# Kernel tuning notes

Measured on AMD Instinct MI355X. Metric: run time of the kernel, lower is better.

## Reference

```python
import jax, jax.numpy as jnp
import numpy as np

B, D, N, H = 16, 512, 4096, 4
HD = D // H  # head_dim = 128


def conv1(x, w, b):
    # 1x1 Conv1d == per-position matmul. x: (b, Cin, L), w: (Cout, Cin), b: (Cout,)
    return jnp.einsum('oi,bin->bon', w, x) + b[:, None]


def ln_c(x, g, b, eps=1e-5):
    # TransLN: LayerNorm over the channel axis (axis=1) at every position.
    m = jnp.mean(x, axis=1, keepdims=True)
    v = jnp.var(x, axis=1, keepdims=True)
    return (x - m) * jax.lax.rsqrt(v + eps) * g[:, None] + b[:, None]


def gelu(x):
    return jax.nn.gelu(x, approximate=False)  # torch nn.GELU default = exact erf


def setup_inputs() -> dict:
    key = jax.random.key(0)
    ks = iter(jax.random.split(key, 40))

    def rn(*shape):
        return jax.random.normal(next(ks), shape, jnp.float32) * 0.02

    inp = {
        'group_token': jax.random.normal(next(ks), (B, D, 2), jnp.float32),
        'x': jax.random.normal(next(ks), (B, D, N), jnp.float32),
        # mlp_s: Mlp(2, D//2) -> Conv1d(2, D//2), GELU, Conv1d(D//2, 2)
        'ws1_w': rn(D // 2, 2), 'ws1_b': jnp.zeros(D // 2, jnp.float32),
        'ws2_w': rn(2, D // 2), 'ws2_b': jnp.zeros(2, jnp.float32),
        # mlp_c: Mlp(D, 4D)
        'wc1_w': rn(4 * D, D), 'wc1_b': jnp.zeros(4 * D, jnp.float32),
        'wc2_w': rn(D, 4 * D), 'wc2_b': jnp.zeros(D, jnp.float32),
        # proj q/k/v: Conv1d(D, D)
        'q_w': rn(D, D), 'q_b': jnp.zeros(D, jnp.float32),
        'k_w': rn(D, D), 'k_b': jnp.zeros(D, jnp.float32),
        'v_w': rn(D, D), 'v_b': jnp.zeros(D, jnp.float32),
        'merge_w': rn(D, D), 'merge_b': jnp.zeros(D, jnp.float32),
        # mlp = MLP([2D, 2D, D], do_bn=False): Conv1d(2D,2D), GELU, Conv1d(2D,D)
        'm1_w': rn(2 * D, 2 * D), 'm1_b': jnp.zeros(2 * D, jnp.float32),
        'm2_w': rn(D, 2 * D), 'm2_b': jnp.zeros(D, jnp.float32),
        # norm0 / norm1 LayerNorm(D)
        'n0_g': jnp.ones(D, jnp.float32), 'n0_b': jnp.zeros(D, jnp.float32),
        'n1_g': jnp.ones(D, jnp.float32), 'n1_b': jnp.zeros(D, jnp.float32),
        # grouping: D->64->16->4->2 with TransLN+GELU between, softmax(axis=1)
        'g1_w': rn(64, D), 'g1_b': jnp.zeros(64, jnp.float32),
        'gl1_g': jnp.ones(64, jnp.float32), 'gl1_b': jnp.zeros(64, jnp.float32),
        'g2_w': rn(16, 64), 'g2_b': jnp.zeros(16, jnp.float32),
        'gl2_g': jnp.ones(16, jnp.float32), 'gl2_b': jnp.zeros(16, jnp.float32),
        'g3_w': rn(4, 16), 'g3_b': jnp.zeros(4, jnp.float32),
        'gl3_g': jnp.ones(4, jnp.float32), 'gl3_b': jnp.zeros(4, jnp.float32),
        'g4_w': rn(2, 4), 'g4_b': jnp.zeros(2, jnp.float32),
    }
    return inp


def reference(group_token, x, ws1_w, ws1_b, ws2_w, ws2_b, wc1_w, wc1_b, wc2_w, wc2_b,
              q_w, q_b, k_w, k_b, v_w, v_b, merge_w, merge_b,
              m1_w, m1_b, m2_w, m2_b, n0_g, n0_b, n1_g, n1_b,
              g1_w, g1_b, gl1_g, gl1_b, g2_w, g2_b, gl2_g, gl2_b,
              g3_w, g3_b, gl3_g, gl3_b, g4_w, g4_b):
    b = x.shape[0]
    # group_token: (b, D, 2)
    gt_t = jnp.swapaxes(group_token, 1, 2)                    # (b, 2, D)
    s = conv1(gelu(conv1(gt_t, ws1_w, ws1_b)), ws2_w, ws2_b)  # (b, 2, D)
    gt = group_token + jnp.swapaxes(s, 1, 2)
    gt = gt + conv1(gelu(conv1(gt, wc1_w, wc1_b)), wc2_w, wc2_b)

    # projections; torch view(b, head_dim, heads, -1) splits channels as (HD, H)
    q = conv1(x, q_w, q_b).reshape(b, HD, H, N)
    k = conv1(gt, k_w, k_b).reshape(b, HD, H, 2)
    v = conv1(gt, v_w, v_b).reshape(b, HD, H, 2)

    attn = jax.nn.softmax(jnp.einsum('bdhn,bdhm->bhnm', q, k) * (HD ** -0.5), axis=-1)
    out = jnp.einsum('bhnm,bdhm->bdhn', attn, v).reshape(b, D, N)
    out = conv1(out, merge_w, merge_b)

    h = jnp.concatenate([x, ln_c(out, n0_g, n0_b)], axis=1)   # (b, 2D, N)
    h = conv1(gelu(conv1(h, m1_w, m1_b)), m2_w, m2_b)         # (b, D, N)
    xd = x + ln_c(h, n1_g, n1_b)

    g = gelu(ln_c(conv1(xd, g1_w, g1_b), gl1_g, gl1_b))
    g = gelu(ln_c(conv1(g, g2_w, g2_b), gl2_g, gl2_b))
    g = gelu(ln_c(conv1(g, g3_w, g3_b), gl3_g, gl3_b))
    g = jax.nn.softmax(conv1(g, g4_w, g4_b), axis=1)          # (b, 2, N)
    return g[:, 0, :]                                         # (b, N)
```

## Files before the change

kernel.cpp:

```cpp
#include <hip/hip_runtime.h>
#include <math.h>

typedef unsigned short u16;
typedef unsigned int u32;
typedef __attribute__((ext_vector_type(8))) short bfrag;
typedef __attribute__((ext_vector_type(4))) float f32x4;

__device__ __forceinline__ float gelu_f(float x){
  float z = fabsf(x) * 0.70710678118654752440f;
  float t = __builtin_amdgcn_rcpf(1.0f + 0.3275911f*z);
  float p = t*(0.254829592f + t*(-0.284496736f + t*(1.421413741f
            + t*(-1.453152027f + t*1.061405429f))));
  float e = __expf(-z*z);
  float er = copysignf(1.0f - p*e, x);
  return 0.5f * x * (1.0f + er);
}
__device__ __forceinline__ u16 f2bf(float f){
  union { float f; unsigned int i; } c; c.f = f;
  unsigned int i = c.i;
  return (u16)((i + 0x7FFFu + ((i >> 16) & 1u)) >> 16);
}
__device__ __forceinline__ float bf2f(u16 u){
  union { unsigned int i; float f; } c; c.i = ((unsigned int)u) << 16; return c.f;
}

__device__ __forceinline__ void gload_lds16(const u16* g, u16* l){
  __builtin_amdgcn_global_load_lds(
      (const __attribute__((address_space(1))) u32*)(g),
      (__attribute__((address_space(3))) u32*)(l),
      16, 0, 0);
}

struct F8 { float v[8]; };
__device__ __forceinline__ F8 load8f(const float* p){
  float4 a = *(const float4*)p; float4 b = *(const float4*)(p + 4);
  F8 r; r.v[0]=a.x; r.v[1]=a.y; r.v[2]=a.z; r.v[3]=a.w;
  r.v[4]=b.x; r.v[5]=b.y; r.v[6]=b.z; r.v[7]=b.w; return r;
}

#define PRE_STRIDE 4624

__global__ __launch_bounds__(256) void k0a_mlps(
    const float* __restrict__ gtok,
    const float* __restrict__ ws1_w, const float* __restrict__ ws1_b,
    const float* __restrict__ ws2_w, const float* __restrict__ ws2_b,
    float* __restrict__ GT1)
{
  __shared__ float sw1[256][2]; __shared__ float sb1[256];
  __shared__ float sw2[2][256];
  const int b = blockIdx.x;
  const int t = threadIdx.x;
  sw1[t][0] = ws1_w[2*t]; sw1[t][1] = ws1_w[2*t+1];
  sb1[t] = ws1_b[t];
  sw2[0][t] = ws2_w[t]; sw2[1][t] = ws2_w[256+t];
  __syncthreads();
  const int j = blockIdx.y*256 + t;
  const float a0 = gtok[b*1024 + 2*j], a1 = gtok[b*1024 + 2*j + 1];
  float s0 = ws2_b[0], s1 = ws2_b[1];
  #pragma unroll 4
  for (int o = 0; o < 256; ++o){
    float h = gelu_f(sw1[o][0]*a0 + sw1[o][1]*a1 + sb1[o]);
    s0 += sw2[0][o]*h; s1 += sw2[1][o]*h;
  }
  GT1[b*1024 + 2*j]     = a0 + s0;
  GT1[b*1024 + 2*j + 1] = a1 + s1;
}

__global__ __launch_bounds__(256) void k0b_fc1(
    const float* __restrict__ GT1,
    const float* __restrict__ wc1_w, const float* __restrict__ wc1_b,
    float* __restrict__ HID)
{
  __shared__ float g[1024];
  const int b = blockIdx.x;
  const int t = threadIdx.x;
  for (int i = t; i < 1024; i += 256) g[i] = GT1[b*1024 + i];
  __syncthreads();
  const int o = blockIdx.y*256 + t;
  const float* wr = wc1_w + (size_t)o*512;
  float acc0 = wc1_b[o], acc1 = acc0;
  for (int d = 0; d < 512; d += 8){
    F8 w = load8f(wr + d);
    #pragma unroll
    for (int i = 0; i < 8; ++i){
      acc0 += w.v[i]*g[(d+i)*2];
      acc1 += w.v[i]*g[(d+i)*2+1];
    }
  }
  HID[b*4096 + o]        = gelu_f(acc0);
  HID[b*4096 + 2048 + o] = gelu_f(acc1);
}

__global__ __launch_bounds__(256) void k0c_fc2(
    const float* __restrict__ GT1, const float* __restrict__ HID,
    const float* __restrict__ wc2_w, const float* __restrict__ wc2_b,
    float* __restrict__ GT2)
{
  __shared__ float h0[2048], h1[2048];
  const int b = blockIdx.x;
  const int t = threadIdx.x;
  for (int i = t; i < 2048; i += 256){
    h0[i] = HID[b*4096 + i]; h1[i] = HID[b*4096 + 2048 + i];
  }
  __syncthreads();
  const int d = blockIdx.y*256 + t;
  const float* wr = wc2_w + (size_t)d*2048;
  float acc0 = wc2_b[d], acc1 = acc0;
  for (int o = 0; o < 2048; o += 8){
    F8 w = load8f(wr + o);
    #pragma unroll
    for (int i = 0; i < 8; ++i){
      acc0 += w.v[i]*h0[o+i];
      acc1 += w.v[i]*h1[o+i];
    }
  }
  GT2[b*1024 + 2*d]     = GT1[b*1024 + 2*d]     + acc0;
  GT2[b*1024 + 2*d + 1] = GT1[b*1024 + 2*d + 1] + acc1;
}

__global__ __launch_bounds__(256) void k0d_kv(
    const float* __restrict__ GT2,
    const float* __restrict__ k_w,
    const float* __restrict__ v_w, const float* __restrict__ v_b,
    float* __restrict__ DK, float* __restrict__ DV, float* __restrict__ V1L)
{
  __shared__ float g[1024];
  const int b = blockIdx.x;
  const int t = threadIdx.x;
  for (int i = t; i < 1024; i += 256) g[i] = GT2[b*1024 + i];
  __syncthreads();
  const int c = blockIdx.y*256 + t;
  const float* kr = k_w + (size_t)c*512;
  const float* vr = v_w + (size_t)c*512;
  float k0a=0.f,k1a=0.f,v0a=0.f,v1a=0.f;
  for (int d = 0; d < 512; d += 8){
    F8 kw = load8f(kr + d); F8 vw = load8f(vr + d);
    #pragma unroll
    for (int i = 0; i < 8; ++i){
      float g0 = g[(d+i)*2], g1 = g[(d+i)*2+1];
      k0a += kw.v[i]*g0; k1a += kw.v[i]*g1;
      v0a += vw.v[i]*g0; v1a += vw.v[i]*g1;
    }
  }
  DK[b*512 + c]  = k0a - k1a;
  DV[b*512 + c]  = v0a - v1a;
  V1L[b*512 + c] = v1a + v_b[c];
}

__global__ __launch_bounds__(256) void k0e_qpre(
    const float* __restrict__ DK,
    const float* __restrict__ q_w, const float* __restrict__ q_b,
    float* __restrict__ PRE)
{
  __shared__ float dkl[512];
  const int b = blockIdx.x;
  const int t = threadIdx.x;
  for (int i = t; i < 512; i += 256) dkl[i] = DK[b*512 + i];
  __syncthreads();
  const int i = blockIdx.y*256 + t;
  float w0=0.f,w1=0.f,w2=0.f,w3=0.f;
  for (int c = 0; c < 512; c += 4){
    w0 += dkl[c]  *q_w[(size_t)(c)  *512 + i];
    w1 += dkl[c+1]*q_w[(size_t)(c+1)*512 + i];
    w2 += dkl[c+2]*q_w[(size_t)(c+2)*512 + i];
    w3 += dkl[c+3]*q_w[(size_t)(c+3)*512 + i];
  }
  float* P = PRE + (size_t)b * PRE_STRIDE;
  P[0*512+i]=w0; P[1*512+i]=w1; P[2*512+i]=w2; P[3*512+i]=w3;
  if (blockIdx.y == 0 && t < 4){
    float bsum = 0.f;
    for (int c = t; c < 512; c += 4) bsum += dkl[c]*q_b[c];
    P[2048 + t] = bsum;
  }
}

__global__ __launch_bounds__(256) void k0f_mpre(
    const float* __restrict__ DV, const float* __restrict__ V1L,
    const float* __restrict__ merge_w, const float* __restrict__ merge_b,
    float* __restrict__ PRE)
{
  __shared__ float dvl[512], v1ll[512];
  const int b = blockIdx.x;
  const int t = threadIdx.x;
  for (int i = t; i < 512; i += 256){
    dvl[i] = DV[b*512 + i]; v1ll[i] = V1L[b*512 + i];
  }
  __syncthreads();
  const int r = blockIdx.y*256 + t;
  const float* mw = merge_w + (size_t)r*512;
  float ab = merge_b[r];
  float mh[4] = {0.f,0.f,0.f,0.f};
  for (int c = 0; c < 512; c += 8){
    F8 w = load8f(mw + c);
    #pragma unroll
    for (int i = 0; i < 8; ++i){
      ab += w.v[i]*v1ll[c+i];
      mh[i&3] += w.v[i]*dvl[c+i];
    }
  }
  float* P = PRE + (size_t)b * PRE_STRIDE;
  P[2064 + r] = ab;
  *(float4*)&P[2576 + r*4] = make_float4(mh[0],mh[1],mh[2],mh[3]);
}

__global__ __launch_bounds__(256) void kcvt(const float* __restrict__ s,
                                            u16* __restrict__ d, int n8)
{
  int g = blockIdx.x*256 + threadIdx.x;
  if (g >= n8) return;
  F8 v = load8f(s + (size_t)g*8);
  u16 o[8];
  #pragma unroll
  for (int i=0;i<8;++i) o[i] = f2bf(v.v[i]);
  *(uint4*)(d + (size_t)g*8) = *(uint4*)o;
}

__global__ __launch_bounds__(256) void kcvt_dup(const float* __restrict__ g1w,
                                                u16* __restrict__ out)
{
  int idx = blockIdx.x*256 + threadIdx.x;
  int r = idx >> 10, k = idx & 1023;
  out[idx] = f2bf(g1w[r*512 + (k & 511)]);
}

__global__ __launch_bounds__(256) void k1_fused(
    const float* __restrict__ x, const float* __restrict__ PRE,
    const float* __restrict__ n0_g, const float* __restrict__ n0_b,
    int j0_global, u16* __restrict__ XYbT)
{
  __shared__ float wd[4][512];
  __shared__ float bs[512];
  __shared__ float Mm[512][4];
  __shared__ float gam[512], bet[512];
  __shared__ float beta4[4];
  __shared__ float part[4][4][64];
  __shared__ float pstat[2][4][64];
  const int tid = threadIdx.x;
  const int cid = tid & 63;
  const int qtr = tid >> 6;
  const int jl = blockIdx.x*64 + cid;
  const int jg = j0_global + jl;
  const int b = jg >> 12, n = jg & 4095;
  const float* P = PRE + (size_t)b * PRE_STRIDE;
  for (int i = tid; i < 2048; i += 256) wd[i>>9][i&511] = P[i];
  if (tid < 4) beta4[tid] = P[2048 + tid];
  for (int i = tid; i < 512; i += 256){
    bs[i] = P[2064 + i]; gam[i] = n0_g[i]; bet[i] = n0_b[i];
  }
  for (int i = tid; i < 2048; i += 256) Mm[i>>2][i&3] = P[2576 + i];
  __syncthreads();
  const float* xc = x + (size_t)b*2097152 + n;
  u16* col = XYbT + (size_t)jl*1024;
  const int ibase = qtr*128;
  float l0=0.f, l1=0.f, l2=0.f, l3=0.f;
  for (int i0 = 0; i0 < 128; i0 += 32){
    u16 ob[32];
    #pragma unroll
    for (int m = 0; m < 32; ++m){
      int i = ibase + i0 + m;
      float xv = xc[(size_t)i*4096];
      ob[m] = f2bf(xv);
      l0 += wd[0][i]*xv; l1 += wd[1][i]*xv;
      l2 += wd[2][i]*xv; l3 += wd[3][i]*xv;
    }
    #pragma unroll
    for (int q = 0; q < 4; ++q)
      *(uint4*)&col[ibase + i0 + 8*q] = *(uint4*)&ob[8*q];
  }
  part[0][qtr][cid] = l0; part[1][qtr][cid] = l1;
  part[2][qtr][cid] = l2; part[3][qtr][cid] = l3;
  __syncthreads();
  l0 = part[0][0][cid] + part[0][1][cid] + part[0][2][cid] + part[0][3][cid] + beta4[0];
  l1 = part[1][0][cid] + part[1][1][cid] + part[1][2][cid] + part[1][3][cid] + beta4[1];
  l2 = part[2][0][cid] + part[2][1][cid] + part[2][2][cid] + part[2][3][cid] + beta4[2];
  l3 = part[3][0][cid] + part[3][1][cid] + part[3][2][cid] + part[3][3][cid] + beta4[3];
  const float sc = 0.0883883476483184405f;
  float p0 = 1.f/(1.f+expf(-sc*l0));
  float p1 = 1.f/(1.f+expf(-sc*l1));
  float p2 = 1.f/(1.f+expf(-sc*l2));
  float p3 = 1.f/(1.f+expf(-sc*l3));
  float s=0.f, s2=0.f;
  for (int c = ibase; c < ibase + 128; ++c){
    float m = bs[c] + Mm[c][0]*p0 + Mm[c][1]*p1 + Mm[c][2]*p2 + Mm[c][3]*p3;
    s += m; s2 += m*m;
  }
  pstat[0][qtr][cid] = s; pstat[1][qtr][cid] = s2;
  __syncthreads();
  s  = pstat[0][0][cid] + pstat[0][1][cid] + pstat[0][2][cid] + pstat[0][3][cid];
  s2 = pstat[1][0][cid] + pstat[1][1][cid] + pstat[1][2][cid] + pstat[1][3][cid];
  float mean = s*(1.f/512.f);
  float rs = rsqrtf(s2*(1.f/512.f) - mean*mean + 1e-5f);
  for (int c0 = 0; c0 < 128; c0 += 32){
    u16 ob[32];
    #pragma unroll
    for (int m = 0; m < 32; ++m){
      int c = ibase + c0 + m;
      float v = bs[c] + Mm[c][0]*p0 + Mm[c][1]*p1 + Mm[c][2]*p2 + Mm[c][3]*p3;
      ob[m] = f2bf((v - mean)*rs*gam[c] + bet[c]);
    }
    #pragma unroll
    for (int q = 0; q < 4; ++q)
      *(uint4*)&col[512 + ibase + c0 + 8*q] = *(uint4*)&ob[8*q];
  }
}

__global__ __launch_bounds__(512) void mfma_gemm_p(
    const u16* __restrict__ Wb, const float* __restrict__ bias,
    const u16* __restrict__ XT, int K, int M,
    u16* __restrict__ Out, int do_gelu, int log2nbi)
{
  __shared__ __align__(16) u16 SH[3][8192];
  const int tid = threadIdx.x;
  const int lane = tid & 63;
  const int wv = __builtin_amdgcn_readfirstlane(tid >> 6);
  const int id = blockIdx.x;
  const int bi = (id >> 3) & ((1 << log2nbi) - 1);
  const int bj = (id & 7) + 8 * (id >> (3 + log2nbi));
  const int roff = (wv >> 2) * 64;
  const int noff = (wv & 3) * 32;
  const int lm = lane & 15, quad = lane >> 4;
  const int qs = (quad ^ ((lm >> 1) & 3)) * 8;

  f32x4 acc[4][2];
  #pragma unroll
  for (int i=0;i<4;++i){
    #pragma unroll
    for (int j=0;j<2;++j) acc[i][j] = (f32x4){0.f,0.f,0.f,0.f};
  }

  const int r16 = lane >> 2;
  const int kc  = (((lane & 3) ^ ((lane >> 3) & 3))) * 8;
  const u16* aG = Wb + (size_t)(bi*128 + wv*16 + r16)*K + kc;
  const u16* bG = XT + (size_t)(bj*128 + wv*16 + r16)*1024 + kc;
  const int aOff = wv*512;
  const int bOff = 4096 + wv*512;

#define GP_STAGE(base, kk) do { \
    gload_lds16(aG + (kk), (base) + aOff); \
    gload_lds16(bG + (kk), (base) + bOff); \
  } while(0)

#define GP_COMPUTE(base) do { \
    bfrag av[4], bv[2]; \
    _Pragma("unroll") \
    for (int i=0;i<4;++i) \
      av[i] = *(const bfrag*)&(base)[(roff + 16*i + lm)*32 + qs]; \
    _Pragma("unroll") \
    for (int j=0;j<2;++j) \
      bv[j] = *(const bfrag*)&(base)[4096 + (noff + 16*j + lm)*32 + qs]; \
    __builtin_amdgcn_s_setprio(1); \
    _Pragma("unroll") \
    for (int i=0;i<4;++i){ \
      _Pragma("unroll") \
      for (int j=0;j<2;++j) \
        acc[i][j] = __builtin_amdgcn_mfma_f32_16x16x32_bf16(av[i], bv[j], acc[i][j], 0,0,0); \
    } \
    __builtin_amdgcn_s_setprio(0); \
  } while(0)

  u16* b0 = &SH[0][0];
  u16* b1 = &SH[1][0];
  u16* b2 = &SH[2][0];
  GP_STAGE(b0, 0);
  GP_STAGE(b1, 32);
  for (int k0 = 0; k0 + 64 < K; k0 += 32){
    GP_STAGE(b2, k0 + 64);
    asm volatile("s_waitcnt vmcnt(4)" ::: "memory");
    __builtin_amdgcn_s_barrier();
    __builtin_amdgcn_sched_barrier(0);
    GP_COMPUTE(b0);
    __builtin_amdgcn_sched_barrier(0);
    __builtin_amdgcn_s_barrier();
    u16* t = b0; b0 = b1; b1 = b2; b2 = t;
  }
  asm volatile("s_waitcnt vmcnt(2)" ::: "memory");
  __builtin_amdgcn_s_barrier();
  __builtin_amdgcn_sched_barrier(0);
  GP_COMPUTE(b0);
  asm volatile("s_waitcnt vmcnt(0)" ::: "memory");
  __builtin_amdgcn_s_barrier();
  __builtin_amdgcn_sched_barrier(0);
  GP_COMPUTE(b1);
  __syncthreads();
#undef GP_STAGE
#undef GP_COMPUTE

  u16* Tt = &SH[0][0];
  #pragma unroll
  for (int i=0;i<4;++i){
    float4 bb = *(const float4*)&bias[bi*128 + roff + 16*i + quad*4];
    float b4[4] = {bb.x,bb.y,bb.z,bb.w};
    #pragma unroll
    for (int j=0;j<2;++j){
      int colr = noff + 16*j + lm;
      #pragma unroll
      for (int s2=0;s2<2;++s2){
        float v0 = acc[i][j][2*s2]   + b4[2*s2];
        float v1 = acc[i][j][2*s2+1] + b4[2*s2+1];
        if (do_gelu){ v0 = gelu_f(v0); v1 = gelu_f(v1); }
        unsigned int dw = (unsigned int)f2bf(v0) | ((unsigned int)f2bf(v1) << 16);
        *(unsigned int*)&Tt[colr*136 + roff + 16*i + quad*4 + 2*s2] = dw;
      }
    }
  }
  __syncthreads();
  {
    int c = tid >> 2, q = tid & 3;
    u16* dst = Out + (size_t)(bj*128 + c)*M + bi*128 + q*32;
    const u16* src = &Tt[c*136 + q*32];
    #pragma unroll
    for (int m=0;m<2;++m){
      *(uint4*)(dst + m*8)      = *(const uint4*)(src + m*8);
      *(uint4*)(dst + 16 + m*8) = *(const uint4*)(src + 16 + m*8);
    }
  }
}

__global__ __launch_bounds__(256) void mfma_g64h(
    const u16* __restrict__ Wg, const float* __restrict__ bias,
    const u16* __restrict__ XT,
    const float* __restrict__ gl1_g, const float* __restrict__ gl1_b,
    const float* __restrict__ g2_w, const float* __restrict__ g2_b,
    const float* __restrict__ gl2_g, const float* __restrict__ gl2_b,
    const float* __restrict__ g3_w, const float* __restrict__ g3_b,
    const float* __restrict__ gl3_g, const float* __restrict__ gl3_b,
    const float* __restrict__ g4_w, const float* __restrict__ g4_b, int has_g4b,
    float* __restrict__ Outp, int j0_global)
{
  __shared__ __align__(16) u16 SH[3][6144];
  const int tid = threadIdx.x;
  const int lane = tid & 63;
  const int wv = __builtin_amdgcn_readfirstlane(tid >> 6);
  const int bj = blockIdx.x;
  const int lm = lane & 15, quad = lane >> 4;
  const int qs = (quad ^ ((lm >> 1) & 3)) * 8;

  f32x4 acc[4][2];
  #pragma unroll
  for (int i=0;i<4;++i){
    #pragma unroll
    for (int j=0;j<2;++j) acc[i][j] = (f32x4){0.f,0.f,0.f,0.f};
  }
  const int r16 = lane >> 2;
  const int kc  = (((lane & 3) ^ ((lane >> 3) & 3))) * 8;
  const u16* aG = Wg + (size_t)(wv*16 + r16)*1024 + kc;
  const u16* bG = XT + (size_t)(bj*128 + wv*32 + r16)*1024 + kc;
  const int aOff = wv*512;
  const int bOff = 2048 + wv*1024;

#define G64_STAGE(base, kk) do { \
    gload_lds16(aG + (kk),             (base) + aOff); \
    gload_lds16(bG + (kk),             (base) + bOff); \
    gload_lds16(bG + 16*1024 + (kk),   (base) + bOff + 512); \
  } while(0)

#define G64_COMPUTE(base) do { \
    bfrag av[4], bv[2]; \
    _Pragma("unroll") \
    for (int i=0;i<4;++i) \
      av[i] = *(const bfrag*)&(base)[(16*i + lm)*32 + qs]; \
    _Pragma("unroll") \
    for (int j=0;j<2;++j) \
      bv[j] = *(const bfrag*)&(base)[2048 + (wv*32 + 16*j + lm)*32 + qs]; \
    __builtin_amdgcn_s_setprio(1); \
    _Pragma("unroll") \
    for (int i=0;i<4;++i){ \
      _Pragma("unroll") \
      for (int j=0;j<2;++j) \
        acc[i][j] = __builtin_amdgcn_mfma_f32_16x16x32_bf16(av[i], bv[j], acc[i][j], 0,0,0); \
    } \
    __builtin_amdgcn_s_setprio(0); \
  } while(0)

  u16* b0 = &SH[0][0];
  u16* b1 = &SH[1][0];
  u16* b2 = &SH[2][0];
  G64_STAGE(b0, 0);
  G64_STAGE(b1, 32);
  for (int k0 = 0; k0 + 64 < 1024; k0 += 32){
    G64_STAGE(b2, k0 + 64);
    asm volatile("s_waitcnt vmcnt(6)" ::: "memory");
    __builtin_amdgcn_s_barrier();
    __builtin_amdgcn_sched_barrier(0);
    G64_COMPUTE(b0);
    __builtin_amdgcn_sched_barrier(0);
    __builtin_amdgcn_s_barrier();
    u16* t = b0; b0 = b1; b1 = b2; b2 = t;
  }
  asm volatile("s_waitcnt vmcnt(3)" ::: "memory");
  __builtin_amdgcn_s_barrier();
  __builtin_amdgcn_sched_barrier(0);
  G64_COMPUTE(b0);
  asm volatile("s_waitcnt vmcnt(0)" ::: "memory");
  __builtin_amdgcn_s_barrier();
  __builtin_amdgcn_sched_barrier(0);
  G64_COMPUTE(b1);
  __syncthreads();
#undef G64_STAGE
#undef G64_COMPUTE

  u16* Tg = &SH[0][0];
  #pragma unroll
  for (int i=0;i<4;++i){
    float4 bb = *(const float4*)&bias[16*i + quad*4];
    float b4[4] = {bb.x,bb.y,bb.z,bb.w};
    #pragma unroll
    for (int j=0;j<2;++j){
      int col = wv*32 + 16*j + lm;
      #pragma unroll
      for (int s2=0;s2<2;++s2){
        float v0 = acc[i][j][2*s2]   + b4[2*s2];
        float v1 = acc[i][j][2*s2+1] + b4[2*s2+1];
        unsigned int dw = (unsigned int)f2bf(v0) | ((unsigned int)f2bf(v1) << 16);
        *(unsigned int*)&Tg[col*72 + 16*i + quad*4 + 2*s2] = dw;
      }
    }
  }
  float* HW = (float*)(&SH[0][0] + 9216);
  if (tid < 64){ HW[tid] = gl1_g[tid]; HW[64+tid] = gl1_b[tid]; }
  for (int i = tid; i < 1024; i += 256) HW[128+i] = g2_w[i];
  if (tid < 16){ HW[1152+tid]=g2_b[tid]; HW[1168+tid]=gl2_g[tid]; HW[1184+tid]=gl2_b[tid]; }
  if (tid >= 64 && tid < 128) HW[1200 + tid-64] = g3_w[tid-64];
  if (tid >= 128 && tid < 132){
    int q = tid - 128;
    HW[1264+q]=g3_b[q]; HW[1268+q]=gl3_g[q]; HW[1272+q]=gl3_b[q];
    HW[1276+q] = g4_w[q] - g4_w[4+q];
  }
  if (tid == 132) HW[1280] = has_g4b ? (g4_b[0] - g4_b[1]) : 0.f;
  __syncthreads();

  if (tid < 128){
    const u16* gc = &Tg[tid*72];
    float a1[64]; float s=0.f;
    #pragma unroll
    for (int c0=0;c0<64;c0+=8){
      uint4 w = *(const uint4*)(gc + c0);
      const u16* wp = (const u16*)&w;
      #pragma unroll
      for (int m=0;m<8;++m){ a1[c0+m] = bf2f(wp[m]); s += a1[c0+m]; }
    }
    float m = s*(1.f/64.f); float s2=0.f;
    #pragma unroll
    for (int c=0;c<64;++c){ float d=a1[c]-m; s2+=d*d; }
    float rs = rsqrtf(s2*(1.f/64.f)+1e-5f);
    #pragma unroll
    for (int c=0;c<64;++c) a1[c] = gelu_f((a1[c]-m)*rs*HW[c]+HW[64+c]);

    float a2[16]; s=0.f;
    #pragma unroll
    for (int i=0;i<16;++i){
      float acc2 = HW[1152+i];
      #pragma unroll
      for (int o=0;o<64;++o) acc2 += HW[128 + i*64 + o]*a1[o];
      a2[i]=acc2; s+=acc2;
    }
    m = s*(1.f/16.f); s2=0.f;
    #pragma unroll
    for (int i=0;i<16;++i){ float d=a2[i]-m; s2+=d*d; }
    rs = rsqrtf(s2*(1.f/16.f)+1e-5f);
    float a2g[16];
    #pragma unroll
    for (int i=0;i<16;++i) a2g[i] = gelu_f((a2[i]-m)*rs*HW[1168+i]+HW[1184+i]);

    float a3[4]; s=0.f;
    #pragma unroll
    for (int i=0;i<4;++i){
      float acc3 = HW[1264+i];
      #pragma unroll
      for (int o=0;o<16;++o) acc3 += HW[1200 + i*16 + o]*a2g[o];
      a3[i]=acc3; s+=acc3;
    }
    m = s*0.25f; s2=0.f;
    #pragma unroll
    for (int i=0;i<4;++i){ float d=a3[i]-m; s2+=d*d; }
    rs = rsqrtf(s2*0.25f+1e-5f);
    float z = HW[1280];
    #pragma unroll
    for (int i=0;i<4;++i) z += HW[1276+i]*gelu_f((a3[i]-m)*rs*HW[1268+i]+HW[1272+i]);
    Outp[j0_global + bj*128 + tid] = 1.f/(1.f+expf(-z));
  }
}

__global__ __launch_bounds__(256) void k_lnT(
    const u16* __restrict__ t2T,
    const float* __restrict__ gamma, const float* __restrict__ beta,
    u16* __restrict__ XYbT)
{
  __shared__ float gam[512], bet[512];
  const int tid = threadIdx.x;
  for (int c = tid; c < 512; c += 256){ gam[c]=gamma[c]; bet[c]=beta[c]; }
  __syncthreads();
  const int lane = tid & 63, wv = tid >> 6;
  const int j = blockIdx.x*4 + wv;
  uint4 w = *(const uint4*)(t2T + (size_t)j*512 + lane*8);
  const u16* wp = (const u16*)&w;
  float vv[8];
  #pragma unroll
  for (int m=0;m<8;++m) vv[m] = bf2f(wp[m]);
  float s = 0.f, s2 = 0.f;
  #pragma unroll
  for (int m=0;m<8;++m){ s += vv[m]; s2 += vv[m]*vv[m]; }
  #pragma unroll
  for (int off = 32; off; off >>= 1){
    s  += __shfl_xor(s,  off, 64);
    s2 += __shfl_xor(s2, off, 64);
  }
  float mean = s*(1.f/512.f);
  float rs = rsqrtf(s2*(1.f/512.f) - mean*mean + 1e-5f);
  u16 ob[8];
  #pragma unroll
  for (int m=0;m<8;++m){
    int c = lane*8 + m;
    ob[m] = f2bf((vv[m]-mean)*rs*gam[c] + bet[c]);
  }
  *(uint4*)&XYbT[(size_t)j*1024 + 512 + lane*8] = *(uint4*)ob;
}

extern "C" void kernel_launch(void* const* d_in, const int* in_sizes, int n_in,
                              void* d_out, int out_size, void* d_ws, size_t ws_size,
                              hipStream_t stream)
{
  const float* gtok  = (const float*)d_in[0];
  const float* x     = (const float*)d_in[1];
  const float* ws1_w = (const float*)d_in[2];
  const float* ws1_b = (const float*)d_in[3];
  const float* ws2_w = (const float*)d_in[4];
  const float* ws2_b = (const float*)d_in[5];
  const float* wc1_w = (const float*)d_in[6];
  const float* wc1_b = (const float*)d_in[7];
  const float* wc2_w = (const float*)d_in[8];
  const float* wc2_b = (const float*)d_in[9];
  const float* q_w   = (const float*)d_in[10];
  const float* q_b   = (const float*)d_in[11];
  const float* k_w   = (const float*)d_in[12];
  const float* v_w   = (const float*)d_in[14];
  const float* v_b   = (const float*)d_in[15];
  const float* merge_w = (const float*)d_in[16];
  const float* merge_b = (const float*)d_in[17];
  const float* m1_w  = (const float*)d_in[18];
  const float* m1_b  = (const float*)d_in[19];
  const float* m2_w  = (const float*)d_in[20];
  const float* m2_b  = (const float*)d_in[21];
  const float* n0_g  = (const float*)d_in[22];
  const float* n0_b  = (const float*)d_in[23];
  const float* n1_g  = (const float*)d_in[24];
  const float* n1_b  = (const float*)d_in[25];
  const float* g1_w  = (const float*)d_in[26];
  const float* g1_b  = (const float*)d_in[27];
  const float* gl1_g = (const float*)d_in[28];
  const float* gl1_b = (const float*)d_in[29];
  const float* g2_w  = (const float*)d_in[30];
  const float* g2_b  = (const float*)d_in[31];
  const float* gl2_g = (const float*)d_in[32];
  const float* gl2_b = (const float*)d_in[33];
  const float* g3_w  = (const float*)d_in[34];
  const float* g3_b  = (const float*)d_in[35];
  const float* gl3_g = (const float*)d_in[36];
  const float* gl3_b = (const float*)d_in[37];
  const float* g4_w  = (const float*)d_in[38];
  const float* g4_b  = (n_in > 39) ? (const float*)d_in[39] : nullptr;

  const int TOT = 65536;
  const size_t PRE_BYTES = (size_t)16 * PRE_STRIDE * 4;
  const size_t GT1_B = 65536, HID_B = 262144, GT2_B = 65536;
  const size_t DK_B = 32768, DV_B = 32768, V1L_B = 32768;
  const size_t WB1_B = (size_t)1024*1024*2;
  const size_t WB2_B = (size_t)512*1024*2;
  const size_t WG_B  = (size_t)64*1024*2;
  const size_t FIXED = PRE_BYTES + GT1_B + HID_B + GT2_B + DK_B + DV_B + V1L_B
                     + WB1_B + WB2_B + WG_B;
  int C = 65536;
  while (C > 4096 && FIXED + (size_t)5120*C > ws_size) C >>= 1;
  const int nch = TOT / C;

  char* wsb = (char*)d_ws;
  size_t off = 0;
  float* PRE = (float*)(wsb + off); off += PRE_BYTES;
  float* GT1 = (float*)(wsb + off); off += GT1_B;
  float* HID = (float*)(wsb + off); off += HID_B;
  float* GT2 = (float*)(wsb + off); off += GT2_B;
  float* DK  = (float*)(wsb + off); off += DK_B;
  float* DV  = (float*)(wsb + off); off += DV_B;
  float* V1L = (float*)(wsb + off); off += V1L_B;
  u16* Wb1   = (u16*)(wsb + off);   off += WB1_B;
  u16* Wb2   = (u16*)(wsb + off);   off += WB2_B;
  u16* Wg    = (u16*)(wsb + off);   off += WG_B;
  u16* XYbT  = (u16*)(wsb + off);   off += (size_t)2048*C;
  u16* T1bT  = (u16*)(wsb + off);   off += (size_t)2048*C;
  u16* T2bT  = (u16*)(wsb + off);   off += (size_t)1024*C;

  dim3 blk(256);
  dim3 blk5(512);
  hipLaunchKernelGGL(kcvt, dim3(512), blk, 0, stream, m1_w, Wb1, 1024*1024/8);
  hipLaunchKernelGGL(kcvt, dim3(256), blk, 0, stream, m2_w, Wb2, 512*1024/8);
  hipLaunchKernelGGL(kcvt_dup, dim3(256), blk, 0, stream, g1_w, Wg);
  hipLaunchKernelGGL(k0a_mlps, dim3(16,2), blk, 0, stream,
      gtok, ws1_w, ws1_b, ws2_w, ws2_b, GT1);
  hipLaunchKernelGGL(k0b_fc1, dim3(16,8), blk, 0, stream, GT1, wc1_w, wc1_b, HID);
  hipLaunchKernelGGL(k0c_fc2, dim3(16,2), blk, 0, stream, GT1, HID, wc2_w, wc2_b, GT2);
  hipLaunchKernelGGL(k0d_kv,  dim3(16,2), blk, 0, stream, GT2, k_w, v_w, v_b, DK, DV, V1L);
  hipLaunchKernelGGL(k0e_qpre, dim3(16,2), blk, 0, stream, DK, q_w, q_b, PRE);
  hipLaunchKernelGGL(k0f_mpre, dim3(16,2), blk, 0, stream, DV, V1L, merge_w, merge_b, PRE);

  for (int ch = 0; ch < nch; ++ch){
    const int j0 = ch * C;
    hipLaunchKernelGGL(k1_fused, dim3(C/64), blk, 0, stream,
        x, PRE, n0_g, n0_b, j0, XYbT);
    hipLaunchKernelGGL(mfma_gemm_p, dim3(8*(C/128)), blk5, 0, stream,
        Wb1, m1_b, XYbT, 1024, 1024, T1bT, 1, 3);
    hipLaunchKernelGGL(mfma_gemm_p, dim3(4*(C/128)), blk5, 0, stream,
        Wb2, m2_b, T1bT, 1024, 512, T2bT, 0, 2);
    hipLaunchKernelGGL(k_lnT, dim3(C/4), blk, 0, stream, T2bT, n1_g, n1_b, XYbT);
    hipLaunchKernelGGL(mfma_g64h, dim3(C/128), blk, 0, stream,
        Wg, g1_b, XYbT,
        gl1_g, gl1_b, g2_w, g2_b, gl2_g, gl2_b,
        g3_w, g3_b, gl3_g, gl3_b,
        g4_w, g4_b ? g4_b : g4_w, g4_b ? 1 : 0, (float*)d_out, j0);
  }
}
```

Before: 892.2 us.

## Double-buffer GEMM K-loop in 64-wide chunks with four LDS stages

Restructures the mfma_gemm_p main loop from a three-buffer ring with 32-wide K steps to a ping-pong of two 64-wide chunks, each split across two 16 KB LDS buffers. Each iteration computes two K-slices between barriers, then issues the loads for the next-next chunk. This halves the number of barrier pairs per K and gives longer compute spans between synchronisations. The cost is 64 KB of LDS per block instead of 48 KB, which may lower occupancy, and a shallower effective prefetch distance relative to compute. It also assumes K is a multiple of 64 and at least 128.

```diff
diff --git a/kernel.cpp b/kernel.cpp
--- a/kernel.cpp
+++ b/kernel.cpp
@@ -309,7 +309,7 @@
     const u16* __restrict__ XT, int K, int M,
     u16* __restrict__ Out, int do_gelu, int log2nbi)
 {
-  __shared__ __align__(16) u16 SH[3][8192];
+  __shared__ __align__(16) u16 SH[4][8192];
   const int tid = threadIdx.x;
   const int lane = tid & 63;
   const int wv = __builtin_amdgcn_readfirstlane(tid >> 6);
@@ -330,14 +330,17 @@
 
   const int r16 = lane >> 2;
   const int kc  = (((lane & 3) ^ ((lane >> 3) & 3))) * 8;
-  const u16* aG = Wb + (size_t)(bi*128 + wv*16 + r16)*K + kc;
-  const u16* bG = XT + (size_t)(bj*128 + wv*16 + r16)*1024 + kc;
+  const u16* pa = Wb + (size_t)(bi*128 + wv*16 + r16)*K + kc;
+  const u16* pb = XT + (size_t)(bj*128 + wv*16 + r16)*1024 + kc;
   const int aOff = wv*512;
   const int bOff = 4096 + wv*512;
 
-#define GP_STAGE(base, kk) do { \
-    gload_lds16(aG + (kk), (base) + aOff); \
-    gload_lds16(bG + (kk), (base) + bOff); \
+#define GP_STAGE2(p0, p1) do { \
+    gload_lds16(pa,      (p0) + aOff); \
+    gload_lds16(pb,      (p0) + bOff); \
+    gload_lds16(pa + 32, (p1) + aOff); \
+    gload_lds16(pb + 32, (p1) + bOff); \
+    pa += 64; pb += 64; \
   } while(0)
 
 #define GP_COMPUTE(base) do { \
@@ -358,31 +361,39 @@
     __builtin_amdgcn_s_setprio(0); \
   } while(0)
 
-  u16* b0 = &SH[0][0];
-  u16* b1 = &SH[1][0];
-  u16* b2 = &SH[2][0];
-  GP_STAGE(b0, 0);
-  GP_STAGE(b1, 32);
-  for (int k0 = 0; k0 + 64 < K; k0 += 32){
-    GP_STAGE(b2, k0 + 64);
+  u16* A0 = &SH[0][0];
+  u16* A1 = &SH[1][0];
+  u16* B0 = &SH[2][0];
+  u16* B1 = &SH[3][0];
+  GP_STAGE2(A0, A1);
+  GP_STAGE2(B0, B1);
+  const int NIT = (K >> 6) - 2;
+  for (int it = 0; it < NIT; ++it){
     asm volatile("s_waitcnt vmcnt(4)" ::: "memory");
     __builtin_amdgcn_s_barrier();
     __builtin_amdgcn_sched_barrier(0);
-    GP_COMPUTE(b0);
+    GP_COMPUTE(A0);
+    GP_COMPUTE(A1);
     __builtin_amdgcn_sched_barrier(0);
     __builtin_amdgcn_s_barrier();
-    u16* t = b0; b0 = b1; b1 = b2; b2 = t;
-  }
-  asm volatile("s_waitcnt vmcnt(2)" ::: "memory");
+    __builtin_amdgcn_sched_barrier(0);
+    GP_STAGE2(A0, A1);
+    u16* t;
+    t = A0; A0 = B0; B0 = t;
+    t = A1; A1 = B1; B1 = t;
+  }
+  asm volatile("s_waitcnt vmcnt(4)" ::: "memory");
   __builtin_amdgcn_s_barrier();
   __builtin_amdgcn_sched_barrier(0);
-  GP_COMPUTE(b0);
+  GP_COMPUTE(A0);
+  GP_COMPUTE(A1);
   asm volatile("s_waitcnt vmcnt(0)" ::: "memory");
   __builtin_amdgcn_s_barrier();
   __builtin_amdgcn_sched_barrier(0);
-  GP_COMPUTE(b1);
-  __syncthreads();
-#undef GP_STAGE
+  GP_COMPUTE(B0);
+  GP_COMPUTE(B1);
+  __syncthreads();
+#undef GP_STAGE2
 #undef GP_COMPUTE
 
   u16* Tt = &SH[0][0];
```

Result: no change. 894.7 us (+0.3%).

## Replace 128x128 MFMA GEMM with 256x256 tile, 8-wave ping-pong pipeline

Applied to the files above, without the earlier changes.

The two big MLP GEMMs move from a 128x128 output tile with a triple-buffered K=32 pipeline to a 256x256 tile with double-buffered K=64 stages. Each wave now computes a 128x64 sub-tile (32 accumulators), and global-to-LDS loads are interleaved with half-stage MFMA groups. The aim is to raise arithmetic intensity and cut LDS and global traffic per FLOP. In exchange, register pressure is much higher and the grid is a quarter the size, which may leave CUs underused when the chunk size is small. The epilogue is written in two halves to fit within LDS.

```diff
diff --git a/kernel.cpp b/kernel.cpp
--- a/kernel.cpp
+++ b/kernel.cpp
@@ -304,115 +304,172 @@
   }
 }
 
-__global__ __launch_bounds__(512) void mfma_gemm_p(
+__global__ __launch_bounds__(512) void mfma_gemm8(
     const u16* __restrict__ Wb, const float* __restrict__ bias,
     const u16* __restrict__ XT, int K, int M,
     u16* __restrict__ Out, int do_gelu, int log2nbi)
 {
-  __shared__ __align__(16) u16 SH[3][8192];
+  __shared__ __align__(16) u16 SH[2][32768];
   const int tid = threadIdx.x;
   const int lane = tid & 63;
   const int wv = __builtin_amdgcn_readfirstlane(tid >> 6);
   const int id = blockIdx.x;
-  const int bi = (id >> 3) & ((1 << log2nbi) - 1);
-  const int bj = (id & 7) + 8 * (id >> (3 + log2nbi));
-  const int roff = (wv >> 2) * 64;
-  const int noff = (wv & 3) * 32;
+  const int bi = id & ((1 << log2nbi) - 1);
+  const int bj = id >> log2nbi;
+  const int roff = (wv >> 2) * 128;
+  const int wn = wv & 3;
+  const int noff = wn * 64;
   const int lm = lane & 15, quad = lane >> 4;
   const int qs = (quad ^ ((lm >> 1) & 3)) * 8;
 
-  f32x4 acc[4][2];
+  f32x4 acc[8][4];
   #pragma unroll
-  for (int i=0;i<4;++i){
-    #pragma unroll
-    for (int j=0;j<2;++j) acc[i][j] = (f32x4){0.f,0.f,0.f,0.f};
-  }
+  for (int i=0;i<8;++i){
+    #pragma unroll
+    for (int j=0;j<4;++j) acc[i][j] = (f32x4){0.f,0.f,0.f,0.f};
+  }
+  bfrag av[8], bv[2];
 
   const int r16 = lane >> 2;
   const int kc  = (((lane & 3) ^ ((lane >> 3) & 3))) * 8;
-  const u16* aG = Wb + (size_t)(bi*128 + wv*16 + r16)*K + kc;
-  const u16* bG = XT + (size_t)(bj*128 + wv*16 + r16)*1024 + kc;
-  const int aOff = wv*512;
-  const int bOff = 4096 + wv*512;
-
-#define GP_STAGE(base, kk) do { \
-    gload_lds16(aG + (kk), (base) + aOff); \
-    gload_lds16(bG + (kk), (base) + bOff); \
+  const u16* aG = Wb + (size_t)(bi*256 + wv*32 + r16)*K + kc;
+  const u16* bG = XT + (size_t)(bj*256 + wv*32 + r16)*1024 + kc;
+  const int a16 = 16*K;
+  const int wlo = wv*1024;
+
+#define G8_STGA(lb, ks, koff) do { \
+    gload_lds16(aG + (koff) + (ks)*32,        (lb) + (ks)*8192 + wlo); \
+    gload_lds16(aG + (koff) + (ks)*32 + a16,  (lb) + (ks)*8192 + wlo + 512); \
   } while(0)
-
-#define GP_COMPUTE(base) do { \
-    bfrag av[4], bv[2]; \
-    _Pragma("unroll") \
-    for (int i=0;i<4;++i) \
-      av[i] = *(const bfrag*)&(base)[(roff + 16*i + lm)*32 + qs]; \
-    _Pragma("unroll") \
+#define G8_STGB(lb, ks, koff) do { \
+    gload_lds16(bG + (koff) + (ks)*32,         (lb) + 16384 + (ks)*8192 + wlo); \
+    gload_lds16(bG + (koff) + (ks)*32 + 16384, (lb) + 16384 + (ks)*8192 + wlo + 512); \
+  } while(0)
+#define G8_RAV(lb, ks) do { _Pragma("unroll") \
+    for (int i=0;i<8;++i) \
+      av[i] = *(const bfrag*)&(lb)[(ks)*8192 + (roff + 16*i + lm)*32 + qs]; \
+  } while(0)
+#define G8_RBV(lb, ks, ch) do { _Pragma("unroll") \
     for (int j=0;j<2;++j) \
-      bv[j] = *(const bfrag*)&(base)[4096 + (noff + 16*j + lm)*32 + qs]; \
+      bv[j] = *(const bfrag*)&(lb)[16384 + (ks)*8192 + (noff + (ch)*32 + 16*j + lm)*32 + qs]; \
+  } while(0)
+#define G8_MMA(ch) do { \
     __builtin_amdgcn_s_setprio(1); \
     _Pragma("unroll") \
-    for (int i=0;i<4;++i){ \
+    for (int i=0;i<8;++i){ \
       _Pragma("unroll") \
       for (int j=0;j<2;++j) \
-        acc[i][j] = __builtin_amdgcn_mfma_f32_16x16x32_bf16(av[i], bv[j], acc[i][j], 0,0,0); \
+        acc[i][(ch)*2+j] = __builtin_amdgcn_mfma_f32_16x16x32_bf16(av[i], bv[j], acc[i][(ch)*2+j], 0,0,0); \
     } \
     __builtin_amdgcn_s_setprio(0); \
   } while(0)
-
-  u16* b0 = &SH[0][0];
-  u16* b1 = &SH[1][0];
-  u16* b2 = &SH[2][0];
-  GP_STAGE(b0, 0);
-  GP_STAGE(b1, 32);
-  for (int k0 = 0; k0 + 64 < K; k0 += 32){
-    GP_STAGE(b2, k0 + 64);
+#define G8_SYNC() do { __builtin_amdgcn_s_barrier(); \
+    asm volatile("s_waitcnt lgkmcnt(0)" ::: "memory"); \
+    __builtin_amdgcn_sched_barrier(0); } while(0)
+#define G8_END() do { __builtin_amdgcn_sched_barrier(0); \
+    __builtin_amdgcn_s_barrier(); } while(0)
+
+  u16* cb = &SH[0][0];
+  u16* nb = &SH[1][0];
+  const int KT = K >> 6;
+  G8_STGA(cb, 0, 0);  G8_STGB(cb, 0, 0);
+  G8_STGA(cb, 1, 0);  G8_STGB(cb, 1, 0);
+  G8_STGA(nb, 0, 64); G8_STGB(nb, 0, 64);
+  asm volatile("s_waitcnt vmcnt(4)" ::: "memory");
+  __builtin_amdgcn_s_barrier();
+
+  for (int T = 0; T < KT-2; ++T){
+    const int k1o = (T+1)*64, k2o = (T+2)*64;
+    G8_RAV(cb, 0); G8_RBV(cb, 0, 0);
+    G8_STGA(nb, 1, k1o);
+    G8_SYNC(); G8_MMA(0); G8_END();
+    G8_RBV(cb, 0, 1);
+    G8_STGB(nb, 1, k1o);
+    G8_SYNC(); G8_MMA(1); G8_END();
+    G8_RAV(cb, 1); G8_RBV(cb, 1, 0);
+    G8_STGA(cb, 0, k2o);
+    G8_SYNC(); G8_MMA(0); G8_END();
+    G8_RBV(cb, 1, 1);
+    G8_STGB(cb, 0, k2o);
+    G8_SYNC(); G8_MMA(1);
+    __builtin_amdgcn_sched_barrier(0);
     asm volatile("s_waitcnt vmcnt(4)" ::: "memory");
     __builtin_amdgcn_s_barrier();
+    u16* t = cb; cb = nb; nb = t;
+  }
+  {
+    const int k1o = (KT-1)*64;
+    G8_RAV(cb, 0); G8_RBV(cb, 0, 0);
+    G8_STGA(nb, 1, k1o);
+    G8_SYNC(); G8_MMA(0); G8_END();
+    G8_RBV(cb, 0, 1);
+    G8_STGB(nb, 1, k1o);
+    G8_SYNC(); G8_MMA(1); G8_END();
+    G8_RAV(cb, 1); G8_RBV(cb, 1, 0);
+    G8_SYNC(); G8_MMA(0); G8_END();
+    G8_RBV(cb, 1, 1);
+    G8_SYNC(); G8_MMA(1);
     __builtin_amdgcn_sched_barrier(0);
-    GP_COMPUTE(b0);
-    __builtin_amdgcn_sched_barrier(0);
+    asm volatile("s_waitcnt vmcnt(0)" ::: "memory");
     __builtin_amdgcn_s_barrier();
-    u16* t = b0; b0 = b1; b1 = b2; b2 = t;
-  }
-  asm volatile("s_waitcnt vmcnt(2)" ::: "memory");
-  __builtin_amdgcn_s_barrier();
+  }
+  G8_RAV(nb, 0); G8_RBV(nb, 0, 0);
+  asm volatile("s_waitcnt lgkmcnt(0)" ::: "memory");
   __builtin_amdgcn_sched_barrier(0);
-  GP_COMPUTE(b0);
-  asm volatile("s_waitcnt vmcnt(0)" ::: "memory");
-  __builtin_amdgcn_s_barrier();
+  G8_MMA(0);
+  G8_RBV(nb, 0, 1);
+  asm volatile("s_waitcnt lgkmcnt(0)" ::: "memory");
   __builtin_amdgcn_sched_barrier(0);
-  GP_COMPUTE(b1);
-  __syncthreads();
-#undef GP_STAGE
-#undef GP_COMPUTE
+  G8_MMA(1);
+  G8_RAV(nb, 1); G8_RBV(nb, 1, 0);
+  asm volatile("s_waitcnt lgkmcnt(0)" ::: "memory");
+  __builtin_amdgcn_sched_barrier(0);
+  G8_MMA(0);
+  G8_RBV(nb, 1, 1);
+  asm volatile("s_waitcnt lgkmcnt(0)" ::: "memory");
+  __builtin_amdgcn_sched_barrier(0);
+  G8_MMA(1);
+  __syncthreads();
+#undef G8_STGA
+#undef G8_STGB
+#undef G8_RAV
+#undef G8_RBV
+#undef G8_MMA
+#undef G8_SYNC
+#undef G8_END
 
   u16* Tt = &SH[0][0];
-  #pragma unroll
-  for (int i=0;i<4;++i){
-    float4 bb = *(const float4*)&bias[bi*128 + roff + 16*i + quad*4];
-    float b4[4] = {bb.x,bb.y,bb.z,bb.w};
-    #pragma unroll
-    for (int j=0;j<2;++j){
-      int colr = noff + 16*j + lm;
+  for (int h = 0; h < 2; ++h){
+    if ((wn >> 1) == h){
+      const int cbase = (wn & 1) * 64;
       #pragma unroll
-      for (int s2=0;s2<2;++s2){
-        float v0 = acc[i][j][2*s2]   + b4[2*s2];
-        float v1 = acc[i][j][2*s2+1] + b4[2*s2+1];
-        if (do_gelu){ v0 = gelu_f(v0); v1 = gelu_f(v1); }
-        unsigned int dw = (unsigned int)f2bf(v0) | ((unsigned int)f2bf(v1) << 16);
-        *(unsigned int*)&Tt[colr*136 + roff + 16*i + quad*4 + 2*s2] = dw;
+      for (int i=0;i<8;++i){
+        float4 bb = *(const float4*)&bias[bi*256 + roff + 16*i + quad*4];
+        float b4[4] = {bb.x,bb.y,bb.z,bb.w};
+        #pragma unroll
+        for (int cx=0;cx<4;++cx){
+          int colr = cbase + cx*16 + lm;
+          #pragma unroll
+          for (int s2=0;s2<2;++s2){
+            float v0 = acc[i][cx][2*s2]   + b4[2*s2];
+            float v1 = acc[i][cx][2*s2+1] + b4[2*s2+1];
+            if (do_gelu){ v0 = gelu_f(v0); v1 = gelu_f(v1); }
+            unsigned int dw = (unsigned int)f2bf(v0) | ((unsigned int)f2bf(v1) << 16);
+            *(unsigned int*)&Tt[colr*264 + roff + 16*i + quad*4 + 2*s2] = dw;
+          }
+        }
       }
     }
-  }
-  __syncthreads();
-  {
-    int c = tid >> 2, q = tid & 3;
-    u16* dst = Out + (size_t)(bj*128 + c)*M + bi*128 + q*32;
-    const u16* src = &Tt[c*136 + q*32];
-    #pragma unroll
-    for (int m=0;m<2;++m){
-      *(uint4*)(dst + m*8)      = *(const uint4*)(src + m*8);
-      *(uint4*)(dst + 16 + m*8) = *(const uint4*)(src + 16 + m*8);
-    }
+    __syncthreads();
+    {
+      int c = tid >> 2, q = tid & 3;
+      u16* dst = Out + (size_t)(bj*256 + h*128 + c)*M + bi*256 + q*64;
+      const u16* src = &Tt[c*264 + q*64];
+      #pragma unroll
+      for (int m=0;m<8;++m)
+        *(uint4*)(dst + m*8) = *(const uint4*)(src + m*8);
+    }
+    __syncthreads();
   }
 }
 
@@ -706,10 +763,10 @@
     const int j0 = ch * C;
     hipLaunchKernelGGL(k1_fused, dim3(C/64), blk, 0, stream,
         x, PRE, n0_g, n0_b, j0, XYbT);
-    hipLaunchKernelGGL(mfma_gemm_p, dim3(8*(C/128)), blk5, 0, stream,
-        Wb1, m1_b, XYbT, 1024, 1024, T1bT, 1, 3);
-    hipLaunchKernelGGL(mfma_gemm_p, dim3(4*(C/128)), blk5, 0, stream,
-        Wb2, m2_b, T1bT, 1024, 512, T2bT, 0, 2);
+    hipLaunchKernelGGL(mfma_gemm8, dim3(4*(C/256)), blk5, 0, stream,
+        Wb1, m1_b, XYbT, 1024, 1024, T1bT, 1, 2);
+    hipLaunchKernelGGL(mfma_gemm8, dim3(2*(C/256)), blk5, 0, stream,
+        Wb2, m2_b, T1bT, 1024, 512, T2bT, 0, 1);
     hipLaunchKernelGGL(k_lnT, dim3(C/4), blk, 0, stream, T2bT, n1_g, n1_b, XYbT);
     hipLaunchKernelGGL(mfma_g64h, dim3(C/128), blk, 0, stream,
         Wg, g1_b, XYbT,
```

New measurement: 1.079 ms. 20.9% more time.
